# Performance work log

Measured on AMD Instinct MI355X. Metric: run time of the kernel, lower is better.

## Reference

```python
import jax, jax.numpy as jnp
import numpy as np

B, S, D = 2, 2048, 2048
KVH, QPG, HD = 8, 4, 64          # kv heads, q heads per group, head size
THETA = 1024.0
PARTIAL = 0.5
SOFT_CAP = 50.0
EPS = 1e-5


def setup_inputs() -> dict:
    key = jax.random.key(0)
    ks = jax.random.split(key, 8)
    scale = 0.02
    return {
        "x": jax.random.normal(ks[0], (B, S, D), jnp.float32),
        "wq": jax.random.normal(ks[1], (KVH, QPG, HD, D), jnp.float32) * scale,
        "wk": jax.random.normal(ks[2], (KVH, HD, D), jnp.float32) * scale,
        "wv": jax.random.normal(ks[3], (KVH, HD, D), jnp.float32) * scale,
        "wo": jax.random.normal(ks[4], (D, KVH, QPG, HD), jnp.float32) * scale,
        "qn_w": jnp.ones((HD,), jnp.float32),
        "kn_w": jnp.ones((HD,), jnp.float32),
        "pos_ids": jnp.arange(S, dtype=jnp.int32),
    }


def _rms_norm(t, w):
    var = jnp.mean(jnp.square(t), axis=-1, keepdims=True)
    return t * jax.lax.rsqrt(var + EPS) * w


def _rope_tables(pos_ids):
    half = HD // 2
    rotated_size = int(HD * PARTIAL)
    inv_freq = 1.0 / THETA ** (jnp.arange(0, 2 * half, 2, dtype=jnp.float32) / rotated_size)
    inv_freq = jnp.where(jnp.arange(half) < rotated_size // 2, inv_freq, 0.0)
    freqs = pos_ids.astype(jnp.float32)[:, None] * inv_freq[None, :]   # [S, half]
    emb = jnp.concatenate([freqs, freqs], axis=-1)                      # [S, HD]
    return jnp.cos(emb), jnp.sin(emb)


def _apply_rope(t, cos, sin):
    # t: [..., S, HD]; rotate_half: (x1, x2) -> (-x2, x1)
    half = HD // 2
    x1, x2 = t[..., :half], t[..., half:]
    rot = jnp.concatenate([-x2, x1], axis=-1)
    return t * cos + rot * sin


def reference(x, wq, wk, wv, wo, qn_w, kn_w, pos_ids):
    # QKV projections (GQA)
    q = jnp.einsum("bsd,gphd->bgpsh", x, wq)   # [B,KVH,QPG,S,HD]
    k = jnp.einsum("bsd,ghd->bgsh", x, wk)      # [B,KVH,S,HD]
    v = jnp.einsum("bsd,ghd->bgsh", x, wv)

    # QK-norm (RMS over head dim)
    q = _rms_norm(q, qn_w)
    k = _rms_norm(k, kn_w)

    # partial RoPE
    cos, sin = _rope_tables(pos_ids)            # [S, HD]
    q = _apply_rope(q, cos, sin).astype(x.dtype)
    k = _apply_rope(k, cos, sin).astype(x.dtype)

    # attention in fp32 (upcast_attn) with soft cap and causal mask
    scale = 1.0 / jnp.sqrt(jnp.float32(HD))
    scores = jnp.einsum("bgpsh,bgth->bgpst", q.astype(jnp.float32), k.astype(jnp.float32)) * scale
    scores = SOFT_CAP * jnp.tanh(scores / SOFT_CAP)
    causal = pos_ids[:, None] >= pos_ids[None, :]                    # [S, S]
    scores = jnp.where(causal, scores, jnp.finfo(jnp.float32).min)
    probs = jax.nn.softmax(scores, axis=-1)
    attn = jnp.einsum("bgpst,bgth->bgpsh", probs, v.astype(jnp.float32)).astype(x.dtype)

    # output projection (flatten kv_head x q_heads_per_group -> heads)
    out = jnp.einsum("bgpsh,dgph->bsd", attn, wo)
    return out
```

## Files before the change

### kernel.cpp

```cpp
#include <hip/hip_runtime.h>
#include <stdint.h>

#define S_LEN   2048
#define D_MODEL 2048
#define N_KVH   8
#define N_QPG   4
#define N_HD    64

typedef __attribute__((ext_vector_type(8)))  short short8;
typedef __attribute__((ext_vector_type(4)))  short short4v;
typedef __attribute__((ext_vector_type(4)))  float float4v;
typedef __attribute__((ext_vector_type(16))) float floatx16;

__device__ __forceinline__ unsigned short f2bf(float x) {
    unsigned int u = __float_as_uint(x);
    u = (u + 0x7fffu + ((u >> 16) & 1u)) >> 16;
    return (unsigned short)u;
}

__device__ __forceinline__ void gload_lds16(const unsigned short* g, unsigned short* l) {
    __builtin_amdgcn_global_load_lds((const __attribute__((address_space(1))) unsigned int*)g,
                                     (__attribute__((address_space(3))) unsigned int*)l,
                                     16, 0, 0);
}

__global__ __launch_bounds__(256) void cvt_all(const float* __restrict__ x,
                                               const float* __restrict__ wq,
                                               const float* __restrict__ wk,
                                               const float* __restrict__ wv,
                                               const float* __restrict__ wo,
                                               unsigned short* __restrict__ xb,
                                               unsigned short* __restrict__ wqb,
                                               unsigned short* __restrict__ wkb,
                                               unsigned short* __restrict__ wvb,
                                               unsigned short* __restrict__ wob) {
    size_t i = (size_t)blockIdx.x * 256 + threadIdx.x;
    const float* src; unsigned short* dst; size_t off;
    if      (i < 1048576) { src = x;  dst = xb;  off = i; }
    else if (i < 1572864) { src = wq; dst = wqb; off = i - 1048576; }
    else if (i < 1703936) { src = wk; dst = wkb; off = i - 1572864; }
    else if (i < 1835008) { src = wv; dst = wvb; off = i - 1703936; }
    else                  { src = wo; dst = wob; off = i - 1835008; }
    const float4* p = (const float4*)src + off * 2;
    float4 a = p[0], b = p[1];
    union { unsigned short us[8]; uint4 v; } u;
    u.us[0] = f2bf(a.x); u.us[1] = f2bf(a.y); u.us[2] = f2bf(a.z); u.us[3] = f2bf(a.w);
    u.us[4] = f2bf(b.x); u.us[5] = f2bf(b.y); u.us[6] = f2bf(b.z); u.us[7] = f2bf(b.w);
    ((uint4*)dst)[off] = u.v;
}

#define GSTAGE(AL, BL, KO)                         \
    gload_lds16(Ag + (KO),          (AL));         \
    gload_lds16(Ag + 16 * K + (KO), (AL) + 512);   \
    gload_lds16(Bg + (KO),          (BL));         \
    gload_lds16(Bg + 16 * K + (KO), (BL) + 512);

#define GCOMPUTE(OFF)                                                          \
    {                                                                          \
        short8 af[4], bf[4];                                                   \
        _Pragma("unroll")                                                      \
        for (int mt = 0; mt < 4; mt++)                                         \
            af[mt] = *(const short8*)(Alds + (OFF) + (wm + mt * 16 + l15) * 32 + quad * 8); \
        _Pragma("unroll")                                                      \
        for (int nt = 0; nt < 4; nt++)                                         \
            bf[nt] = *(const short8*)(Blds + (OFF) + (wn + nt * 16 + l15) * 32 + quad * 8); \
        _Pragma("unroll")                                                      \
        for (int mt = 0; mt < 4; mt++)                                         \
            _Pragma("unroll")                                                  \
            for (int nt = 0; nt < 4; nt++)                                     \
                acc[mt][nt] = __builtin_amdgcn_mfma_f32_16x16x32_bf16(         \
                    af[mt], bf[nt], acc[mt][nt], 0, 0, 0);                     \
    }

__global__ __launch_bounds__(256)
void gemm_qkv(const unsigned short* __restrict__ xb,
              const unsigned short* __restrict__ wqb,
              const unsigned short* __restrict__ wkb,
              const unsigned short* __restrict__ wvb,
              unsigned short* __restrict__ qout,
              unsigned short* __restrict__ kout,
              unsigned short* __restrict__ vtout,
              const float* __restrict__ qnw,
              const float* __restrict__ knw)
{
    __shared__ __align__(16) unsigned short Alds[2 * 128 * 32];
    __shared__ __align__(16) unsigned short Blds[2 * 128 * 32];

    const int tid  = threadIdx.x;
    const int lane = tid & 63;
    const int wave = tid >> 6;
    const int quad = lane >> 4;
    const int l15  = lane & 15;
    const int bx = blockIdx.x, by = blockIdx.y;
    const int role = (by < 16) ? 0 : (by < 20 ? 1 : 2);
    const unsigned short* A;
    const unsigned short* B;
    int m0, n0;
    if (role == 0)      { A = xb;  B = wqb; m0 = bx * 128; n0 = by * 128; }
    else if (role == 1) { A = xb;  B = wkb; m0 = bx * 128; n0 = (by - 16) * 128; }
    else                { A = wvb; B = xb;  m0 = (by - 20) * 128; n0 = bx * 128; }
    const int K = 2048;
    const int wm = (wave >> 1) * 64;
    const int wn = (wave & 1) * 64;

    float4v acc[4][4];
#pragma unroll
    for (int i = 0; i < 4; i++)
#pragma unroll
        for (int j = 0; j < 4; j++) acc[i][j] = (float4v){0.f, 0.f, 0.f, 0.f};

    const int j0 = wave * 2;
    const int lr = lane >> 2;
    const int lc = (lane & 3) * 8;
    const unsigned short* Ag = A + (size_t)(m0 + j0 * 16 + lr) * K + lc;
    const unsigned short* Bg = B + (size_t)(n0 + j0 * 16 + lr) * K + lc;
    unsigned short* Al0 = Alds + j0 * 512;
    unsigned short* Bl0 = Blds + j0 * 512;
    unsigned short* Al1 = Alds + 4096 + j0 * 512;
    unsigned short* Bl1 = Blds + 4096 + j0 * 512;

    GSTAGE(Al0, Bl0, 0);
    __syncthreads();

    for (int k0 = 0; k0 < K; k0 += 64) {
        GSTAGE(Al1, Bl1, k0 + 32);
        GCOMPUTE(0);
        __syncthreads();
        if (k0 + 64 < K) { GSTAGE(Al0, Bl0, k0 + 64); }
        GCOMPUTE(4096);
        __syncthreads();
    }

    const int nb = n0 + wn;
    const float* nw = (role == 1) ? knw : qnw;
#pragma unroll
    for (int mt = 0; mt < 4; mt++) {
#pragma unroll
        for (int r = 0; r < 4; r++) {
            const int m = m0 + wm + mt * 16 + quad * 4 + r;
            if (role == 2) {
#pragma unroll
                for (int nt = 0; nt < 4; nt++) {
                    int n = nb + nt * 16 + l15;
                    vtout[((size_t)(n >> 11) * 512 + m) * 2048 + (n & 2047)] =
                        f2bf(acc[mt][nt][r]);
                }
            } else {
                float v0 = acc[mt][0][r], v1 = acc[mt][1][r], v2 = acc[mt][2][r], v3 = acc[mt][3][r];
                float s2 = v0 * v0 + v1 * v1 + v2 * v2 + v3 * v3;
#pragma unroll
                for (int off = 1; off < 16; off <<= 1) s2 += __shfl_xor(s2, off, 64);
                float rs = rsqrtf(s2 * (1.0f / 64.0f) + 1e-5f);
                float nv0 = v0 * rs * nw[0 * 16 + l15];
                float nv1 = v1 * rs * nw[1 * 16 + l15];
                float nv2 = v2 * rs * nw[2 * 16 + l15];
                float nv3 = v3 * rs * nw[3 * 16 + l15];
                const int bidx = m >> 11, s = m & 2047;
                float ang = (float)s * exp2f(-0.625f * (float)l15);
                float sn, cs;
                __sincosf(ang, &sn, &cs);
                float o0 = nv0 * cs - nv2 * sn;
                float o2 = nv2 * cs + nv0 * sn;
                unsigned short* dst;
                if (role == 0) {
                    const int g = nb >> 8, p = (nb >> 6) & 3;
                    dst = qout + ((((size_t)bidx * N_KVH + g) * N_QPG + p) * S_LEN + s) * N_HD;
                } else {
                    const int g = nb >> 6;
                    dst = kout + (((size_t)bidx * N_KVH + g) * S_LEN + s) * N_HD;
                }
                dst[0 * 16 + l15] = f2bf(o0);
                dst[1 * 16 + l15] = f2bf(nv1);
                dst[2 * 16 + l15] = f2bf(o2);
                dst[3 * 16 + l15] = f2bf(nv3);
            }
        }
    }
}

__global__ __launch_bounds__(256)
void gemm_out(const unsigned short* __restrict__ A,
              const unsigned short* __restrict__ B,
              float* __restrict__ C,
              int M, int N, int K)
{
    __shared__ __align__(16) unsigned short Alds[2 * 128 * 32];
    __shared__ __align__(16) unsigned short Blds[2 * 128 * 32];

    const int tid  = threadIdx.x;
    const int lane = tid & 63;
    const int wave = tid >> 6;
    const int quad = lane >> 4;
    const int l15  = lane & 15;
    const int m0 = blockIdx.x * 128;
    const int n0 = blockIdx.y * 128;
    const int wm = (wave >> 1) * 64;
    const int wn = (wave & 1) * 64;

    float4v acc[4][4];
#pragma unroll
    for (int i = 0; i < 4; i++)
#pragma unroll
        for (int j = 0; j < 4; j++) acc[i][j] = (float4v){0.f, 0.f, 0.f, 0.f};

    const int j0 = wave * 2;
    const int lr = lane >> 2;
    const int lc = (lane & 3) * 8;
    const unsigned short* Ag = A + (size_t)(m0 + j0 * 16 + lr) * K + lc;
    const unsigned short* Bg = B + (size_t)(n0 + j0 * 16 + lr) * K + lc;
    unsigned short* Al0 = Alds + j0 * 512;
    unsigned short* Bl0 = Blds + j0 * 512;
    unsigned short* Al1 = Alds + 4096 + j0 * 512;
    unsigned short* Bl1 = Blds + 4096 + j0 * 512;

    GSTAGE(Al0, Bl0, 0);
    __syncthreads();

    for (int k0 = 0; k0 < K; k0 += 64) {
        GSTAGE(Al1, Bl1, k0 + 32);
        GCOMPUTE(0);
        __syncthreads();
        if (k0 + 64 < K) { GSTAGE(Al0, Bl0, k0 + 64); }
        GCOMPUTE(4096);
        __syncthreads();
    }

    const int nb = n0 + wn;
#pragma unroll
    for (int mt = 0; mt < 4; mt++) {
#pragma unroll
        for (int r = 0; r < 4; r++) {
            const int m = m0 + wm + mt * 16 + quad * 4 + r;
#pragma unroll
            for (int nt = 0; nt < 4; nt++) {
                int n = nb + nt * 16 + l15;
                C[(size_t)m * N + n] = acc[mt][nt][r];
            }
        }
    }
}

__global__ __launch_bounds__(256)
void attn_kernel(const unsigned short* __restrict__ Q,
                 const unsigned short* __restrict__ Kb,
                 const unsigned short* __restrict__ Vt,
                 unsigned short* __restrict__ O)
{
    const int tid  = threadIdx.x;
    const int lane = tid & 63;
    const int w    = tid >> 6;
    const int l31  = lane & 31;
    const int hi   = lane >> 5;
    const int hi8  = hi * 8;
    const int hi4  = hi * 4;
    const bool lo  = (hi == 0);
    const int qx = blockIdx.y;
    const int bg = blockIdx.x;
    const int b = bg >> 3, g = bg & 7;

    const unsigned short* qbase  = Q  + (((size_t)b * N_KVH + g) * N_QPG + w) * S_LEN * N_HD;
    const unsigned short* kbase  = Kb + ((size_t)b * N_KVH + g) * S_LEN * N_HD;
    const unsigned short* vtbase = Vt + ((size_t)b * N_KVH + g) * (size_t)N_HD * S_LEN;

    for (int half = 0; half < 2; half++) {
        const int qt = half ? (63 - qx) : qx;
        const int qrow0 = qt * 32;
        const int ktend = qt;

        short8 qf[4];
#pragma unroll
        for (int c = 0; c < 4; c++)
            qf[c] = *(const short8*)(qbase + (size_t)(qrow0 + l31) * N_HD + c * 16 + hi8);

        floatx16 o_acc[2];
#pragma unroll
        for (int dt = 0; dt < 2; dt++)
#pragma unroll
            for (int i = 0; i < 16; i++) o_acc[dt][i] = 0.f;
        float rsum = 0.f;

        short8 kf[4];
#pragma unroll
        for (int c = 0; c < 4; c++)
            kf[c] = *(const short8*)(kbase + (size_t)(l31) * N_HD + c * 16 + hi8);

        for (int kt = 0; kt <= ktend; kt++) {
            floatx16 s;
#pragma unroll
            for (int i = 0; i < 16; i++) s[i] = 0.f;
            __builtin_amdgcn_s_setprio(1);
#pragma unroll
            for (int c = 0; c < 4; c++)
                s = __builtin_amdgcn_mfma_f32_32x32x16_bf16(kf[c], qf[c], s, 0, 0, 0);
            __builtin_amdgcn_s_setprio(0);

            short8 vf00 = *(const short8*)(vtbase + (size_t)(l31)      * S_LEN + kt * 32 + hi8);
            short8 vf01 = *(const short8*)(vtbase + (size_t)(l31)      * S_LEN + kt * 32 + 16 + hi8);
            short8 vf10 = *(const short8*)(vtbase + (size_t)(32 + l31) * S_LEN + kt * 32 + hi8);
            short8 vf11 = *(const short8*)(vtbase + (size_t)(32 + l31) * S_LEN + kt * 32 + 16 + hi8);

            if (kt < ktend) {
#pragma unroll
                for (int c = 0; c < 4; c++)
                    kf[c] = *(const short8*)(kbase + (size_t)((kt + 1) * 32 + l31) * N_HD + c * 16 + hi8);
            }

            const bool diag = (kt == ktend);
            float p[16];
#pragma unroll
            for (int r = 0; r < 16; r++) {
                float a = s[r];
                float u = a * a;
                float wv = fmaf(u, -3.757018e-7f, 0.18033688f);
                float pv = __builtin_amdgcn_exp2f(fmaf(a, wv, -72.13475204f));
                if (diag) {
                    int kl = (r & 3) + 8 * (r >> 2) + hi4;
                    pv = (kl <= l31) ? pv : 0.0f;
                }
                rsum += pv;
                p[r] = pv;
            }

            unsigned X0, X1, Y0, Y1, Z0, Z1, W0, W1;
            asm("v_cvt_pk_bf16_f32 %0, %1, %2" : "=v"(X0) : "v"(p[0]),  "v"(p[1]));
            asm("v_cvt_pk_bf16_f32 %0, %1, %2" : "=v"(X1) : "v"(p[2]),  "v"(p[3]));
            asm("v_cvt_pk_bf16_f32 %0, %1, %2" : "=v"(Y0) : "v"(p[4]),  "v"(p[5]));
            asm("v_cvt_pk_bf16_f32 %0, %1, %2" : "=v"(Y1) : "v"(p[6]),  "v"(p[7]));
            asm("v_cvt_pk_bf16_f32 %0, %1, %2" : "=v"(Z0) : "v"(p[8]),  "v"(p[9]));
            asm("v_cvt_pk_bf16_f32 %0, %1, %2" : "=v"(Z1) : "v"(p[10]), "v"(p[11]));
            asm("v_cvt_pk_bf16_f32 %0, %1, %2" : "=v"(W0) : "v"(p[12]), "v"(p[13]));
            asm("v_cvt_pk_bf16_f32 %0, %1, %2" : "=v"(W1) : "v"(p[14]), "v"(p[15]));
            unsigned sX0 = (unsigned)__shfl_xor((int)X0, 32, 64);
            unsigned sX1 = (unsigned)__shfl_xor((int)X1, 32, 64);
            unsigned sY0 = (unsigned)__shfl_xor((int)Y0, 32, 64);
            unsigned sY1 = (unsigned)__shfl_xor((int)Y1, 32, 64);
            unsigned sZ0 = (unsigned)__shfl_xor((int)Z0, 32, 64);
            unsigned sZ1 = (unsigned)__shfl_xor((int)Z1, 32, 64);
            unsigned sW0 = (unsigned)__shfl_xor((int)W0, 32, 64);
            unsigned sW1 = (unsigned)__shfl_xor((int)W1, 32, 64);
            union { unsigned u[4]; short8 s8; } pb0, pb1;
            pb0.u[0] = lo ? X0  : sY0;
            pb0.u[1] = lo ? X1  : sY1;
            pb0.u[2] = lo ? sX0 : Y0;
            pb0.u[3] = lo ? sX1 : Y1;
            pb1.u[0] = lo ? Z0  : sW0;
            pb1.u[1] = lo ? Z1  : sW1;
            pb1.u[2] = lo ? sZ0 : W0;
            pb1.u[3] = lo ? sZ1 : W1;

            __builtin_amdgcn_s_setprio(1);
            o_acc[0] = __builtin_amdgcn_mfma_f32_32x32x16_bf16(vf00, pb0.s8, o_acc[0], 0, 0, 0);
            o_acc[0] = __builtin_amdgcn_mfma_f32_32x32x16_bf16(vf01, pb1.s8, o_acc[0], 0, 0, 0);
            o_acc[1] = __builtin_amdgcn_mfma_f32_32x32x16_bf16(vf10, pb0.s8, o_acc[1], 0, 0, 0);
            o_acc[1] = __builtin_amdgcn_mfma_f32_32x32x16_bf16(vf11, pb1.s8, o_acc[1], 0, 0, 0);
            __builtin_amdgcn_s_setprio(0);
        }

        rsum += __shfl_xor(rsum, 32, 64);
        float inv = 1.0f / rsum;
        size_t rowoff = ((size_t)(b * S_LEN + qrow0 + l31)) * D_MODEL + (g * N_QPG + w) * N_HD;
#pragma unroll
        for (int dt = 0; dt < 2; dt++) {
#pragma unroll
            for (int gg = 0; gg < 4; gg++) {
                union { unsigned short us[4]; unsigned long long v; } pk;
#pragma unroll
                for (int j = 0; j < 4; j++)
                    pk.us[j] = f2bf(o_acc[dt][gg * 4 + j] * inv);
                *(unsigned long long*)(O + rowoff + dt * 32 + gg * 8 + hi4) = pk.v;
            }
        }
    }
}

extern "C" void kernel_launch(void* const* d_in, const int* in_sizes, int n_in,
                              void* d_out, int out_size, void* d_ws, size_t ws_size,
                              hipStream_t stream)
{
    const float* x    = (const float*)d_in[0];
    const float* wq   = (const float*)d_in[1];
    const float* wk   = (const float*)d_in[2];
    const float* wv   = (const float*)d_in[3];
    const float* wo   = (const float*)d_in[4];
    const float* qn_w = (const float*)d_in[5];
    const float* kn_w = (const float*)d_in[6];

    char* ws = (char*)d_ws;
    unsigned short* xb  = (unsigned short*)(ws + 0);
    unsigned short* wqb = (unsigned short*)(ws + 16777216);
    unsigned short* wkb = (unsigned short*)(ws + 25165824);
    unsigned short* wvb = (unsigned short*)(ws + 27262976);
    unsigned short* wob = (unsigned short*)(ws + 29360128);
    unsigned short* qb  = (unsigned short*)(ws + 37748736);
    unsigned short* kb  = (unsigned short*)(ws + 54525952);
    unsigned short* vt  = (unsigned short*)(ws + 58720256);
    unsigned short* ab  = (unsigned short*)(ws + 62914560);

    cvt_all<<<dim3(9216), 256, 0, stream>>>(x, wq, wk, wv, wo, xb, wqb, wkb, wvb, wob);

    gemm_qkv<<<dim3(32, 24), 256, 0, stream>>>(xb, wqb, wkb, wvb, qb, kb, vt, qn_w, kn_w);

    attn_kernel<<<dim3(16, 32), 256, 0, stream>>>(qb, kb, vt, ab);

    gemm_out<<<dim3(32, 16), 256, 0, stream>>>(ab, wob, (float*)d_out, 4096, 2048, 2048);
}
```

Before: 380.0 us.

## Split attention KV range across two wave groups and reduce partials in LDS

The attention block grows from 256 to 512 threads. Two wave groups each process half of the causal key tiles for the same query tile, and the second group's partial output accumulators and row sums are combined with the first group's through shared memory before normalisation and store. This doubles the parallelism per query tile and shortens each wave's serial key loop. In exchange it adds 32KB of LDS, two barriers per half, and the reduction traffic, and it may lower occupancy.

Result: no change. 380.9 us (+0.2%).

```diff
diff --git a/kernel.cpp b/kernel.cpp
--- a/kernel.cpp
+++ b/kernel.cpp
@@ -240,15 +240,20 @@
     }
 }
 
-__global__ __launch_bounds__(256)
+__global__ __launch_bounds__(512)
 void attn_kernel(const unsigned short* __restrict__ Q,
                  const unsigned short* __restrict__ Kb,
                  const unsigned short* __restrict__ Vt,
                  unsigned short* __restrict__ O)
 {
+    __shared__ float Osc[4 * 32 * 64];
+    __shared__ float Rsc[4 * 64];
+
     const int tid  = threadIdx.x;
     const int lane = tid & 63;
-    const int w    = tid >> 6;
+    const int wv   = tid >> 6;
+    const int p    = wv & 3;
+    const int kvh  = wv >> 2;
     const int l31  = lane & 31;
     const int hi   = lane >> 5;
     const int hi8  = hi * 8;
@@ -258,14 +263,19 @@
     const int bg = blockIdx.x;
     const int b = bg >> 3, g = bg & 7;
 
-    const unsigned short* qbase  = Q  + (((size_t)b * N_KVH + g) * N_QPG + w) * S_LEN * N_HD;
+    const unsigned short* qbase  = Q  + (((size_t)b * N_KVH + g) * N_QPG + p) * S_LEN * N_HD;
     const unsigned short* kbase  = Kb + ((size_t)b * N_KVH + g) * S_LEN * N_HD;
     const unsigned short* vtbase = Vt + ((size_t)b * N_KVH + g) * (size_t)N_HD * S_LEN;
+
+    float* OscW = Osc + p * (32 * 64);
+    float* RscW = Rsc + p * 64;
 
     for (int half = 0; half < 2; half++) {
         const int qt = half ? (63 - qx) : qx;
         const int qrow0 = qt * 32;
-        const int ktend = qt;
+        const int nkt = qt + 1;
+        const int klo = kvh ? (nkt >> 1) : 0;
+        const int khi = kvh ? nkt : (nkt >> 1);
 
         short8 qf[4];
 #pragma unroll
@@ -279,95 +289,116 @@
             for (int i = 0; i < 16; i++) o_acc[dt][i] = 0.f;
         float rsum = 0.f;
 
-        short8 kf[4];
-#pragma unroll
-        for (int c = 0; c < 4; c++)
-            kf[c] = *(const short8*)(kbase + (size_t)(l31) * N_HD + c * 16 + hi8);
-
-        for (int kt = 0; kt <= ktend; kt++) {
-            floatx16 s;
-#pragma unroll
-            for (int i = 0; i < 16; i++) s[i] = 0.f;
-            __builtin_amdgcn_s_setprio(1);
+        if (klo < khi) {
+            short8 kf[4];
 #pragma unroll
             for (int c = 0; c < 4; c++)
-                s = __builtin_amdgcn_mfma_f32_32x32x16_bf16(kf[c], qf[c], s, 0, 0, 0);
-            __builtin_amdgcn_s_setprio(0);
-
-            short8 vf00 = *(const short8*)(vtbase + (size_t)(l31)      * S_LEN + kt * 32 + hi8);
-            short8 vf01 = *(const short8*)(vtbase + (size_t)(l31)      * S_LEN + kt * 32 + 16 + hi8);
-            short8 vf10 = *(const short8*)(vtbase + (size_t)(32 + l31) * S_LEN + kt * 32 + hi8);
-            short8 vf11 = *(const short8*)(vtbase + (size_t)(32 + l31) * S_LEN + kt * 32 + 16 + hi8);
-
-            if (kt < ktend) {
+                kf[c] = *(const short8*)(kbase + (size_t)(klo * 32 + l31) * N_HD + c * 16 + hi8);
+
+            for (int kt = klo; kt < khi; kt++) {
+                floatx16 s;
+#pragma unroll
+                for (int i = 0; i < 16; i++) s[i] = 0.f;
+                __builtin_amdgcn_s_setprio(1);
 #pragma unroll
                 for (int c = 0; c < 4; c++)
-                    kf[c] = *(const short8*)(kbase + (size_t)((kt + 1) * 32 + l31) * N_HD + c * 16 + hi8);
+                    s = __builtin_amdgcn_mfma_f32_32x32x16_bf16(kf[c], qf[c], s, 0, 0, 0);
+                __builtin_amdgcn_s_setprio(0);
+
+                short8 vf00 = *(const short8*)(vtbase + (size_t)(l31)      * S_LEN + kt * 32 + hi8);
+                short8 vf01 = *(const short8*)(vtbase + (size_t)(l31)      * S_LEN + kt * 32 + 16 + hi8);
+                short8 vf10 = *(const short8*)(vtbase + (size_t)(32 + l31) * S_LEN + kt * 32 + hi8);
+                short8 vf11 = *(const short8*)(vtbase + (size_t)(32 + l31) * S_LEN + kt * 32 + 16 + hi8);
+
+                if (kt + 1 < khi) {
+#pragma unroll
+                    for (int c = 0; c < 4; c++)
+                        kf[c] = *(const short8*)(kbase + (size_t)((kt + 1) * 32 + l31) * N_HD + c * 16 + hi8);
+                }
+
+                const bool diag = (kt == qt);
+                float pr[16];
+#pragma unroll
+                for (int r = 0; r < 16; r++) {
+                    float a = s[r];
+                    float u = a * a;
+                    float wvv = fmaf(u, -3.757018e-7f, 0.18033688f);
+                    float pv = __builtin_amdgcn_exp2f(fmaf(a, wvv, -72.13475204f));
+                    if (diag) {
+                        int kl = (r & 3) + 8 * (r >> 2) + hi4;
+                        pv = (kl <= l31) ? pv : 0.0f;
+                    }
+                    rsum += pv;
+                    pr[r] = pv;
+                }
+
+                unsigned X0, X1, Y0, Y1, Z0, Z1, W0, W1;
+                asm("v_cvt_pk_bf16_f32 %0, %1, %2" : "=v"(X0) : "v"(pr[0]),  "v"(pr[1]));
+                asm("v_cvt_pk_bf16_f32 %0, %1, %2" : "=v"(X1) : "v"(pr[2]),  "v"(pr[3]));
+                asm("v_cvt_pk_bf16_f32 %0, %1, %2" : "=v"(Y0) : "v"(pr[4]),  "v"(pr[5]));
+                asm("v_cvt_pk_bf16_f32 %0, %1, %2" : "=v"(Y1) : "v"(pr[6]),  "v"(pr[7]));
+                asm("v_cvt_pk_bf16_f32 %0, %1, %2" : "=v"(Z0) : "v"(pr[8]),  "v"(pr[9]));
+                asm("v_cvt_pk_bf16_f32 %0, %1, %2" : "=v"(Z1) : "v"(pr[10]), "v"(pr[11]));
+                asm("v_cvt_pk_bf16_f32 %0, %1, %2" : "=v"(W0) : "v"(pr[12]), "v"(pr[13]));
+                asm("v_cvt_pk_bf16_f32 %0, %1, %2" : "=v"(W1) : "v"(pr[14]), "v"(pr[15]));
+                unsigned sX0 = (unsigned)__shfl_xor((int)X0, 32, 64);
+                unsigned sX1 = (unsigned)__shfl_xor((int)X1, 32, 64);
+                unsigned sY0 = (unsigned)__shfl_xor((int)Y0, 32, 64);
+                unsigned sY1 = (unsigned)__shfl_xor((int)Y1, 32, 64);
+                unsigned sZ0 = (unsigned)__shfl_xor((int)Z0, 32, 64);
+                unsigned sZ1 = (unsigned)__shfl_xor((int)Z1, 32, 64);
+                unsigned sW0 = (unsigned)__shfl_xor((int)W0, 32, 64);
+                unsigned sW1 = (unsigned)__shfl_xor((int)W1, 32, 64);
+                union { unsigned u[4]; short8 s8; } pb0, pb1;
+                pb0.u[0] = lo ? X0  : sY0;
+                pb0.u[1] = lo ? X1  : sY1;
+                pb0.u[2] = lo ? sX0 : Y0;
+                pb0.u[3] = lo ? sX1 : Y1;
+                pb1.u[0] = lo ? Z0  : sW0;
+                pb1.u[1] = lo ? Z1  : sW1;
+                pb1.u[2] = lo ? sZ0 : W0;
+                pb1.u[3] = lo ? sZ1 : W1;
+
+                __builtin_amdgcn_s_setprio(1);
+                o_acc[0] = __builtin_amdgcn_mfma_f32_32x32x16_bf16(vf00, pb0.s8, o_acc[0], 0, 0, 0);
+                o_acc[0] = __builtin_amdgcn_mfma_f32_32x32x16_bf16(vf01, pb1.s8, o_acc[0], 0, 0, 0);
+                o_acc[1] = __builtin_amdgcn_mfma_f32_32x32x16_bf16(vf10, pb0.s8, o_acc[1], 0, 0, 0);
+                o_acc[1] = __builtin_amdgcn_mfma_f32_32x32x16_bf16(vf11, pb1.s8, o_acc[1], 0, 0, 0);
+                __builtin_amdgcn_s_setprio(0);
             }
-
-            const bool diag = (kt == ktend);
-            float p[16];
-#pragma unroll
-            for (int r = 0; r < 16; r++) {
-                float a = s[r];
-                float u = a * a;
-                float wv = fmaf(u, -3.757018e-7f, 0.18033688f);
-                float pv = __builtin_amdgcn_exp2f(fmaf(a, wv, -72.13475204f));
-                if (diag) {
-                    int kl = (r & 3) + 8 * (r >> 2) + hi4;
-                    pv = (kl <= l31) ? pv : 0.0f;
+        }
+
+        __syncthreads();
+        if (kvh == 1) {
+#pragma unroll
+            for (int dt = 0; dt < 2; dt++)
+#pragma unroll
+                for (int i = 0; i < 16; i++)
+                    OscW[(dt * 16 + i) * 64 + lane] = o_acc[dt][i];
+            RscW[lane] = rsum;
+        }
+        __syncthreads();
+        if (kvh == 0) {
+#pragma unroll
+            for (int dt = 0; dt < 2; dt++)
+#pragma unroll
+                for (int i = 0; i < 16; i++)
+                    o_acc[dt][i] += OscW[(dt * 16 + i) * 64 + lane];
+            rsum += RscW[lane];
+
+            rsum += __shfl_xor(rsum, 32, 64);
+            float inv = 1.0f / rsum;
+            size_t rowoff = ((size_t)(b * S_LEN + qrow0 + l31)) * D_MODEL + (g * N_QPG + p) * N_HD;
+#pragma unroll
+            for (int dt = 0; dt < 2; dt++) {
+#pragma unroll
+                for (int gg = 0; gg < 4; gg++) {
+                    union { unsigned short us[4]; unsigned long long v; } pk;
+#pragma unroll
+                    for (int j = 0; j < 4; j++)
+                        pk.us[j] = f2bf(o_acc[dt][gg * 4 + j] * inv);
+                    *(unsigned long long*)(O + rowoff + dt * 32 + gg * 8 + hi4) = pk.v;
                 }
-                rsum += pv;
-                p[r] = pv;
-            }
-
-            unsigned X0, X1, Y0, Y1, Z0, Z1, W0, W1;
-            asm("v_cvt_pk_bf16_f32 %0, %1, %2" : "=v"(X0) : "v"(p[0]),  "v"(p[1]));
-            asm("v_cvt_pk_bf16_f32 %0, %1, %2" : "=v"(X1) : "v"(p[2]),  "v"(p[3]));
-            asm("v_cvt_pk_bf16_f32 %0, %1, %2" : "=v"(Y0) : "v"(p[4]),  "v"(p[5]));
-            asm("v_cvt_pk_bf16_f32 %0, %1, %2" : "=v"(Y1) : "v"(p[6]),  "v"(p[7]));
-            asm("v_cvt_pk_bf16_f32 %0, %1, %2" : "=v"(Z0) : "v"(p[8]),  "v"(p[9]));
-            asm("v_cvt_pk_bf16_f32 %0, %1, %2" : "=v"(Z1) : "v"(p[10]), "v"(p[11]));
-            asm("v_cvt_pk_bf16_f32 %0, %1, %2" : "=v"(W0) : "v"(p[12]), "v"(p[13]));
-            asm("v_cvt_pk_bf16_f32 %0, %1, %2" : "=v"(W1) : "v"(p[14]), "v"(p[15]));
-            unsigned sX0 = (unsigned)__shfl_xor((int)X0, 32, 64);
-            unsigned sX1 = (unsigned)__shfl_xor((int)X1, 32, 64);
-            unsigned sY0 = (unsigned)__shfl_xor((int)Y0, 32, 64);
-            unsigned sY1 = (unsigned)__shfl_xor((int)Y1, 32, 64);
-            unsigned sZ0 = (unsigned)__shfl_xor((int)Z0, 32, 64);
-            unsigned sZ1 = (unsigned)__shfl_xor((int)Z1, 32, 64);
-            unsigned sW0 = (unsigned)__shfl_xor((int)W0, 32, 64);
-            unsigned sW1 = (unsigned)__shfl_xor((int)W1, 32, 64);
-            union { unsigned u[4]; short8 s8; } pb0, pb1;
-            pb0.u[0] = lo ? X0  : sY0;
-            pb0.u[1] = lo ? X1  : sY1;
-            pb0.u[2] = lo ? sX0 : Y0;
-            pb0.u[3] = lo ? sX1 : Y1;
-            pb1.u[0] = lo ? Z0  : sW0;
-            pb1.u[1] = lo ? Z1  : sW1;
-            pb1.u[2] = lo ? sZ0 : W0;
-            pb1.u[3] = lo ? sZ1 : W1;
-
-            __builtin_amdgcn_s_setprio(1);
-            o_acc[0] = __builtin_amdgcn_mfma_f32_32x32x16_bf16(vf00, pb0.s8, o_acc[0], 0, 0, 0);
-            o_acc[0] = __builtin_amdgcn_mfma_f32_32x32x16_bf16(vf01, pb1.s8, o_acc[0], 0, 0, 0);
-            o_acc[1] = __builtin_amdgcn_mfma_f32_32x32x16_bf16(vf10, pb0.s8, o_acc[1], 0, 0, 0);
-            o_acc[1] = __builtin_amdgcn_mfma_f32_32x32x16_bf16(vf11, pb1.s8, o_acc[1], 0, 0, 0);
-            __builtin_amdgcn_s_setprio(0);
-        }
-
-        rsum += __shfl_xor(rsum, 32, 64);
-        float inv = 1.0f / rsum;
-        size_t rowoff = ((size_t)(b * S_LEN + qrow0 + l31)) * D_MODEL + (g * N_QPG + w) * N_HD;
-#pragma unroll
-        for (int dt = 0; dt < 2; dt++) {
-#pragma unroll
-            for (int gg = 0; gg < 4; gg++) {
-                union { unsigned short us[4]; unsigned long long v; } pk;
-#pragma unroll
-                for (int j = 0; j < 4; j++)
-                    pk.us[j] = f2bf(o_acc[dt][gg * 4 + j] * inv);
-                *(unsigned long long*)(O + rowoff + dt * 32 + gg * 8 + hi4) = pk.v;
             }
         }
     }
@@ -400,7 +431,7 @@
 
     gemm_qkv<<<dim3(32, 24), 256, 0, stream>>>(xb, wqb, wkb, wvb, qb, kb, vt, qn_w, kn_w);
 
-    attn_kernel<<<dim3(16, 32), 256, 0, stream>>>(qb, kb, vt, ab);
+    attn_kernel<<<dim3(16, 32), 512, 0, stream>>>(qb, kb, vt, ab);
 
     gemm_out<<<dim3(32, 16), 256, 0, stream>>>(ab, wob, (float*)d_out, 4096, 2048, 2048);
 }
```
